# Kernel optimization log

Hardware: AMD Instinct MI355X
Metric: run time of the kernel (lower is better)

The kernel has to match this reference:

```python
import jax, jax.numpy as jnp
import numpy as np

L1 = 512
LX = 32
COUNT = 8


def setup_inputs() -> dict:
    key = jax.random.key(0)
    ks = jax.random.split(key, 9)
    B = 65536
    x = jax.random.uniform(ks[0], (B, 2 * L1), dtype=jnp.float32)  # NNUE accumulator is in [0,1]
    ls_indices = jax.random.randint(ks[1], (B,), 0, COUNT, dtype=jnp.int64)
    # params (scaled ~1/sqrt(fan_in))
    w_fact = jax.random.normal(ks[2], (LX, 2 * L1), dtype=jnp.float32) * (1.0 / np.sqrt(2 * L1))
    w0 = jax.random.normal(ks[3], (LX * COUNT, 2 * L1), dtype=jnp.float32) * (1.0 / np.sqrt(2 * L1))
    b0 = jax.random.normal(ks[4], (LX * COUNT,), dtype=jnp.float32) * 0.05
    w1 = jax.random.normal(ks[5], (LX * COUNT, LX), dtype=jnp.float32) * (1.0 / np.sqrt(LX))
    b1 = jax.random.normal(ks[6], (LX * COUNT,), dtype=jnp.float32) * 0.05
    w2 = jax.random.normal(ks[7], (1 * COUNT, LX), dtype=jnp.float32) * (1.0 / np.sqrt(LX))
    b2 = jax.random.normal(ks[8], (1 * COUNT,), dtype=jnp.float32) * 0.05
    return {"x": x, "ls_indices": ls_indices, "w_fact": w_fact,
            "w0": w0, "b0": b0, "w1": w1, "b1": b1, "w2": w2, "b2": b2}


def _stack_linear_gather(h, w, b, idx, out_dim):
    # dense Linear for all COUNT buckets, then gather the selected bucket per row
    y = (h @ w.T + b).reshape(-1, COUNT, out_dim)          # [B, COUNT, out_dim]
    return y.reshape(-1, out_dim)[idx]                      # [B, out_dim]


def reference(x, ls_indices, w_fact, w0, b0, w1, b1, w2, b2):
    B = x.shape[0]
    idx = ls_indices.astype(jnp.int32) + jnp.arange(B, dtype=jnp.int32) * COUNT
    l1f = x @ w_fact.T                                      # [B, LX]
    h = _stack_linear_gather(x, w0, b0, idx, LX) + l1f      # layer 0 + factorized term
    h = jnp.clip(h, 0.0, 1.0)
    h = _stack_linear_gather(h, w1, b1, idx, LX)            # hidden layer 1
    h = jnp.clip(h, 0.0, 1.0)
    out = _stack_linear_gather(h, w2, b2, idx, 1)           # output layer (no clamp)
    return out
```

## Files before the change

kernel.cpp:

```cpp
#include <hip/hip_runtime.h>


#define B_ROWS 65536
#define LK     1024
#define TILE   32
#define MAIN_BLOCKS (B_ROWS / TILE + 8)
#define SROW   2056

#define SORTED_OFF 1024
#define WB_OFF     (1024 + 131072)

typedef short  short8  __attribute__((ext_vector_type(8)));
typedef float  f32x16  __attribute__((ext_vector_type(16)));

__device__ __forceinline__ unsigned pkbf(float a, float b) {
    unsigned ua = __float_as_uint(a), ub = __float_as_uint(b);
    ua = (ua + 0x7FFFu + ((ua >> 16) & 1u)) >> 16;
    ub = (ub + 0x7FFFu + ((ub >> 16) & 1u)) >> 16;
    return (ua & 0xFFFFu) | (ub << 16);
}

__device__ __forceinline__ bool detect_i64(const int* p) {
    int acc = 0;
#pragma unroll
    for (int i = 0; i < 64; ++i) acc |= p[2 * i + 1];
    return acc == 0;
}

__device__ __forceinline__ int load_bucket(const int* p, int r, bool i64) {
    return (i64 ? p[2 * r] : p[r]) & 7;
}

__global__ __launch_bounds__(1024) void k_prep(
    const int* __restrict__ idx, const float* __restrict__ w0,
    const float* __restrict__ wf, uint4* __restrict__ wB,
    unsigned short* __restrict__ sorted, int* __restrict__ hdr)
{
    int t = threadIdx.x;

    if (blockIdx.x > 0) {
        int f = (blockIdx.x - 1) * 1024 + t;
        int b   = f >> 12;
        int i12 = f & 4095;
        int kc  = i12 >> 8;
        int i8  = i12 & 255;
        int n   = i8 & 31;
        int khi = i8 >> 5;
        int k = kc * 64 + khi * 8;
        const float* p0 = w0 + (size_t)(b * 32 + n) * LK + k;
        const float* pf = wf + (size_t)n * LK + k;
        float v[8];
#pragma unroll
        for (int j = 0; j < 8; ++j) v[j] = p0[j] + pf[j];
        uint4 o;
        o.x = pkbf(v[0], v[1]); o.y = pkbf(v[2], v[3]);
        o.z = pkbf(v[4], v[5]); o.w = pkbf(v[6], v[7]);
        wB[f] = o;
        return;
    }

    __shared__ int wcnt[16][8];
    __shared__ int wbase[16][8];
    __shared__ int segb[8];

    bool i64 = detect_i64(idx);
    int wv = t >> 6, lane = t & 63;
    int rowbase = wv * 4096;

    unsigned nib[8] = {0, 0, 0, 0, 0, 0, 0, 0};
    int c[8] = {0, 0, 0, 0, 0, 0, 0, 0};
#pragma unroll 8
    for (int i = 0; i < 64; ++i) {
        int r = rowbase + i * 64 + lane;
        int b = load_bucket(idx, r, i64);
        nib[i >> 3] |= (unsigned)b << (4 * (i & 7));
#pragma unroll
        for (int bb = 0; bb < 8; ++bb) c[bb] += (b == bb) ? 1 : 0;
    }
#pragma unroll
    for (int bb = 0; bb < 8; ++bb) {
        int v = c[bb];
#pragma unroll
        for (int s = 1; s < 64; s <<= 1) v += __shfl_xor(v, s);
        if (lane == 0) wcnt[wv][bb] = v;
    }
    __syncthreads();

    if (t == 0) {
        int base = 0, tt = 0;
        for (int b = 0; b < 8; ++b) {
            int tot = 0;
            for (int w = 0; w < 16; ++w) tot += wcnt[w][b];
            hdr[b] = tot; hdr[16 + b] = base; hdr[24 + b] = tt;
            segb[b] = base;
            base += tot;
            tt += (tot + TILE - 1) / TILE;
        }
        hdr[24 + 8] = tt;
    }
    __syncthreads();

    if (t < 128) {
        int w2 = t >> 3, b = t & 7;
        int base = segb[b];
        for (int w = 0; w < w2; ++w) base += wcnt[w][b];
        wbase[w2][b] = base;
    }
    __syncthreads();

    int mycur = (lane < 8) ? wbase[wv][lane] : 0;
#pragma unroll
    for (int i = 0; i < 64; ++i) {
        int b = (nib[i >> 3] >> (4 * (i & 7))) & 7;
        unsigned long long mown = 0;
        int addc = 0;
#pragma unroll
        for (int bb = 0; bb < 8; ++bb) {
            unsigned long long m = __ballot(b == bb);
            if (b == bb) mown = m;
            if (lane == bb) addc = __popcll(m);
        }
        int base = __shfl(mycur, b);
        int rank = __popcll(mown & ((1ull << lane) - 1ull));
        sorted[base + rank] = (unsigned short)(rowbase + i * 64 + lane);
        mycur += addc;
    }
}

__global__ __launch_bounds__(256, 2) void k_main(
    const float* __restrict__ x, const unsigned short* __restrict__ sorted,
    const int* __restrict__ hdr, const uint4* __restrict__ wB,
    const float* __restrict__ b0, const float* __restrict__ w1,
    const float* __restrict__ b1, const float* __restrict__ w2,
    const float* __restrict__ b2, float* __restrict__ out)
{
    __shared__ __align__(16) unsigned char smem[TILE * SROW];
    float* rbuf = (float*)smem;
    float* hb   = (float*)(smem + 16384);

    int total = hdr[24 + 8];
    int g = blockIdx.x;
    if (g >= total) return;

    int bkt = 0;
    while (bkt < 7 && hdr[24 + bkt + 1] <= g) bkt++;
    int tile  = g - hdr[24 + bkt];
    int cnt   = hdr[bkt];
    int seg   = hdr[16 + bkt];
    int p0    = seg + tile * TILE;
    int nrows = min(TILE, cnt - tile * TILE);

    int t    = threadIdx.x;
    int lane = t & 63;
    int wv   = t >> 6;

#pragma unroll
    for (int j0 = 0; j0 < 32; j0 += 8) {
        float4 v[8];
#pragma unroll
        for (int jj = 0; jj < 8; ++jj) {
            int j = j0 + jj;
            int gr = (int)sorted[p0 + min(j, nrows - 1)];
            v[jj] = ((const float4*)(x + (size_t)gr * LK))[t];
        }
#pragma unroll
        for (int jj = 0; jj < 8; ++jj) {
            int j = j0 + jj;
            uint2 o;
            o.x = pkbf(v[jj].x, v[jj].y);
            o.y = pkbf(v[jj].z, v[jj].w);
            *(uint2*)(smem + j * SROW + t * 8) = o;
        }
    }
    __syncthreads();

    const uint4* wBg = wB + (size_t)bkt * 4096;
    const unsigned char* Abase = smem + (size_t)(lane & 31) * SROW + 16 * (lane >> 5);

    f32x16 acc;
#pragma unroll
    for (int i = 0; i < 16; ++i) acc[i] = 0.0f;

    union UA { uint2 h[2]; short8 s; };
    union UB { uint4 u;    short8 s; };
#pragma unroll
    for (int cc = 0; cc < 16; ++cc) {
        int c = wv * 16 + cc;
        UA ua;
        ua.h[0] = *(const uint2*)(Abase + 32 * c);
        ua.h[1] = *(const uint2*)(Abase + 32 * c + 8);
        UB ub;
        ub.u = wBg[c * 64 + lane];
        acc = __builtin_amdgcn_mfma_f32_32x32x16_bf16(ua.s, ub.s, acc, 0, 0, 0);
    }

    __syncthreads();
#pragma unroll
    for (int r = 0; r < 16; ++r)
        rbuf[wv * 1024 + r * 64 + lane] = acc[r];
    __syncthreads();

#pragma unroll
    for (int q = 0; q < 4; ++q) {
        int e = t + 256 * q;
        float s = rbuf[e] + rbuf[1024 + e] + rbuf[2048 + e] + rbuf[3072 + e];
        int rr = e >> 6, ll = e & 63;
        int m = (rr & 3) + 8 * (rr >> 2) + 4 * (ll >> 5);
        int n = ll & 31;
        float h = s + b0[bkt * 32 + n];
        h = fminf(fmaxf(h, 0.0f), 1.0f);
        hb[m * 36 + n] = h;
    }
    __syncthreads();

    if (t < 64) {
        int r = t >> 1, half = t & 1;
        const float4* hr = (const float4*)(hb + r * 36);
        float4 ha[8];
#pragma unroll
        for (int q = 0; q < 8; ++q) ha[q] = hr[q];
        const float* w1b = w1 + (size_t)bkt * 1024;
        const float* b1b = b1 + bkt * 32;
        const float* w2b = w2 + bkt * 32;
        float partial = 0.0f;
#pragma unroll
        for (int jj = 0; jj < 16; ++jj) {
            int j2 = half * 16 + jj;
            const float4* wr = (const float4*)&w1b[j2 * 32];
            float s = b1b[j2];
#pragma unroll
            for (int q = 0; q < 8; ++q) {
                float4 w4 = wr[q];
                s += ha[q].x * w4.x + ha[q].y * w4.y + ha[q].z * w4.z + ha[q].w * w4.w;
            }
            s = fminf(fmaxf(s, 0.0f), 1.0f);
            partial += s * w2b[j2];
        }
        partial += __shfl_xor(partial, 1);
        if (half == 0 && r < nrows) {
            int gr = (int)sorted[p0 + r];
            out[gr] = partial + b2[bkt];
        }
    }
}

extern "C" void kernel_launch(void* const* d_in, const int* in_sizes, int n_in,
                              void* d_out, int out_size, void* d_ws, size_t ws_size,
                              hipStream_t stream) {
    const float* x   = (const float*)d_in[0];
    const int*   lsi = (const int*)  d_in[1];
    const float* wf  = (const float*)d_in[2];
    const float* w0  = (const float*)d_in[3];
    const float* b0  = (const float*)d_in[4];
    const float* w1  = (const float*)d_in[5];
    const float* b1  = (const float*)d_in[6];
    const float* w2  = (const float*)d_in[7];
    const float* b2  = (const float*)d_in[8];
    float* out = (float*)d_out;

    char* ws = (char*)d_ws;
    int* hdr = (int*)ws;
    unsigned short* sorted = (unsigned short*)(ws + SORTED_OFF);
    uint4* wB = (uint4*)(ws + WB_OFF);

    k_prep<<<33, 1024, 0, stream>>>(lsi, w0, wf, wB, sorted, hdr);
    k_main<<<MAIN_BLOCKS, 256, 0, stream>>>(x, sorted, hdr, wB,
                                            b0, w1, b1, w2, b2, out);
}
```

Measured before the change: 434.3 us.

## Compute all eight buckets densely per tile instead of sorting rows by bucket

Drops the bucket sort and the indirect row gather. Each block now reads 32 contiguous rows and computes layer 0 for all eight buckets, with each wave handling two buckets over the full K range, so no cross-wave reduction is needed. The per-row bucket then selects which hidden vector feeds the small tail layers, and the tail is spread over all 256 threads instead of 64. This removes the sort pass, the scattered loads and the split-K reduction, at the cost of roughly eight times more MFMA work and more weight reads per block.

```diff
diff --git a/kernel.cpp b/kernel.cpp
--- a/kernel.cpp
+++ b/kernel.cpp
@@ -4,11 +4,8 @@
 #define B_ROWS 65536
 #define LK     1024
 #define TILE   32
-#define MAIN_BLOCKS (B_ROWS / TILE + 8)
+#define NBLK   (B_ROWS / TILE)
 #define SROW   2056
-
-#define SORTED_OFF 1024
-#define WB_OFF     (1024 + 131072)
 
 typedef short  short8  __attribute__((ext_vector_type(8)));
 typedef float  f32x16  __attribute__((ext_vector_type(16)));
@@ -32,216 +29,127 @@
 }
 
 __global__ __launch_bounds__(1024) void k_prep(
-    const int* __restrict__ idx, const float* __restrict__ w0,
-    const float* __restrict__ wf, uint4* __restrict__ wB,
-    unsigned short* __restrict__ sorted, int* __restrict__ hdr)
+    const float* __restrict__ w0, const float* __restrict__ wf,
+    uint4* __restrict__ wB)
 {
-    int t = threadIdx.x;
-
-    if (blockIdx.x > 0) {
-        int f = (blockIdx.x - 1) * 1024 + t;
-        int b   = f >> 12;
-        int i12 = f & 4095;
-        int kc  = i12 >> 8;
-        int i8  = i12 & 255;
-        int n   = i8 & 31;
-        int khi = i8 >> 5;
-        int k = kc * 64 + khi * 8;
-        const float* p0 = w0 + (size_t)(b * 32 + n) * LK + k;
-        const float* pf = wf + (size_t)n * LK + k;
-        float v[8];
+    int f = blockIdx.x * 1024 + threadIdx.x;
+    int b   = f >> 12;
+    int i12 = f & 4095;
+    int kc  = i12 >> 8;
+    int i8  = i12 & 255;
+    int n   = i8 & 31;
+    int khi = i8 >> 5;
+    int k = kc * 64 + khi * 8;
+    const float* p0 = w0 + (size_t)(b * 32 + n) * LK + k;
+    const float* pf = wf + (size_t)n * LK + k;
+    float v[8];
 #pragma unroll
-        for (int j = 0; j < 8; ++j) v[j] = p0[j] + pf[j];
-        uint4 o;
-        o.x = pkbf(v[0], v[1]); o.y = pkbf(v[2], v[3]);
-        o.z = pkbf(v[4], v[5]); o.w = pkbf(v[6], v[7]);
-        wB[f] = o;
-        return;
-    }
-
-    __shared__ int wcnt[16][8];
-    __shared__ int wbase[16][8];
-    __shared__ int segb[8];
-
-    bool i64 = detect_i64(idx);
-    int wv = t >> 6, lane = t & 63;
-    int rowbase = wv * 4096;
-
-    unsigned nib[8] = {0, 0, 0, 0, 0, 0, 0, 0};
-    int c[8] = {0, 0, 0, 0, 0, 0, 0, 0};
-#pragma unroll 8
-    for (int i = 0; i < 64; ++i) {
-        int r = rowbase + i * 64 + lane;
-        int b = load_bucket(idx, r, i64);
-        nib[i >> 3] |= (unsigned)b << (4 * (i & 7));
-#pragma unroll
-        for (int bb = 0; bb < 8; ++bb) c[bb] += (b == bb) ? 1 : 0;
-    }
-#pragma unroll
-    for (int bb = 0; bb < 8; ++bb) {
-        int v = c[bb];
-#pragma unroll
-        for (int s = 1; s < 64; s <<= 1) v += __shfl_xor(v, s);
-        if (lane == 0) wcnt[wv][bb] = v;
-    }
-    __syncthreads();
-
-    if (t == 0) {
-        int base = 0, tt = 0;
-        for (int b = 0; b < 8; ++b) {
-            int tot = 0;
-            for (int w = 0; w < 16; ++w) tot += wcnt[w][b];
-            hdr[b] = tot; hdr[16 + b] = base; hdr[24 + b] = tt;
-            segb[b] = base;
-            base += tot;
-            tt += (tot + TILE - 1) / TILE;
-        }
-        hdr[24 + 8] = tt;
-    }
-    __syncthreads();
-
-    if (t < 128) {
-        int w2 = t >> 3, b = t & 7;
-        int base = segb[b];
-        for (int w = 0; w < w2; ++w) base += wcnt[w][b];
-        wbase[w2][b] = base;
-    }
-    __syncthreads();
-
-    int mycur = (lane < 8) ? wbase[wv][lane] : 0;
-#pragma unroll
-    for (int i = 0; i < 64; ++i) {
-        int b = (nib[i >> 3] >> (4 * (i & 7))) & 7;
-        unsigned long long mown = 0;
-        int addc = 0;
-#pragma unroll
-        for (int bb = 0; bb < 8; ++bb) {
-            unsigned long long m = __ballot(b == bb);
-            if (b == bb) mown = m;
-            if (lane == bb) addc = __popcll(m);
-        }
-        int base = __shfl(mycur, b);
-        int rank = __popcll(mown & ((1ull << lane) - 1ull));
-        sorted[base + rank] = (unsigned short)(rowbase + i * 64 + lane);
-        mycur += addc;
-    }
+    for (int j = 0; j < 8; ++j) v[j] = p0[j] + pf[j];
+    uint4 o;
+    o.x = pkbf(v[0], v[1]); o.y = pkbf(v[2], v[3]);
+    o.z = pkbf(v[4], v[5]); o.w = pkbf(v[6], v[7]);
+    wB[f] = o;
 }
 
 __global__ __launch_bounds__(256, 2) void k_main(
-    const float* __restrict__ x, const unsigned short* __restrict__ sorted,
-    const int* __restrict__ hdr, const uint4* __restrict__ wB,
+    const float* __restrict__ x, const int* __restrict__ idx,
+    const uint4* __restrict__ wB,
     const float* __restrict__ b0, const float* __restrict__ w1,
     const float* __restrict__ b1, const float* __restrict__ w2,
     const float* __restrict__ b2, float* __restrict__ out)
 {
     __shared__ __align__(16) unsigned char smem[TILE * SROW];
-    float* rbuf = (float*)smem;
-    float* hb   = (float*)(smem + 16384);
+    float* hb = (float*)smem;
 
-    int total = hdr[24 + 8];
-    int g = blockIdx.x;
-    if (g >= total) return;
-
-    int bkt = 0;
-    while (bkt < 7 && hdr[24 + bkt + 1] <= g) bkt++;
-    int tile  = g - hdr[24 + bkt];
-    int cnt   = hdr[bkt];
-    int seg   = hdr[16 + bkt];
-    int p0    = seg + tile * TILE;
-    int nrows = min(TILE, cnt - tile * TILE);
-
+    int g    = blockIdx.x;
+    int row0 = g * TILE;
     int t    = threadIdx.x;
     int lane = t & 63;
     int wv   = t >> 6;
 
+    const float4* src = (const float4*)(x + (size_t)row0 * LK);
 #pragma unroll
     for (int j0 = 0; j0 < 32; j0 += 8) {
         float4 v[8];
 #pragma unroll
-        for (int jj = 0; jj < 8; ++jj) {
-            int j = j0 + jj;
-            int gr = (int)sorted[p0 + min(j, nrows - 1)];
-            v[jj] = ((const float4*)(x + (size_t)gr * LK))[t];
-        }
+        for (int jj = 0; jj < 8; ++jj)
+            v[jj] = src[(j0 + jj) * 256 + t];
 #pragma unroll
         for (int jj = 0; jj < 8; ++jj) {
-            int j = j0 + jj;
             uint2 o;
             o.x = pkbf(v[jj].x, v[jj].y);
             o.y = pkbf(v[jj].z, v[jj].w);
-            *(uint2*)(smem + j * SROW + t * 8) = o;
+            *(uint2*)(smem + (j0 + jj) * SROW + t * 8) = o;
         }
     }
     __syncthreads();
 
-    const uint4* wBg = wB + (size_t)bkt * 4096;
-    const unsigned char* Abase = smem + (size_t)(lane & 31) * SROW + 16 * (lane >> 5);
+    const unsigned char* Ab = smem + (size_t)(lane & 31) * SROW + 16 * (lane >> 5);
+    const uint4* wB0 = wB + (size_t)(2 * wv) * 4096;
+    const uint4* wB1 = wB0 + 4096;
 
-    f32x16 acc;
+    f32x16 acc0, acc1;
 #pragma unroll
-    for (int i = 0; i < 16; ++i) acc[i] = 0.0f;
+    for (int i = 0; i < 16; ++i) { acc0[i] = 0.0f; acc1[i] = 0.0f; }
 
     union UA { uint2 h[2]; short8 s; };
     union UB { uint4 u;    short8 s; };
-#pragma unroll
-    for (int cc = 0; cc < 16; ++cc) {
-        int c = wv * 16 + cc;
+#pragma unroll 4
+    for (int c = 0; c < 64; ++c) {
         UA ua;
-        ua.h[0] = *(const uint2*)(Abase + 32 * c);
-        ua.h[1] = *(const uint2*)(Abase + 32 * c + 8);
-        UB ub;
-        ub.u = wBg[c * 64 + lane];
-        acc = __builtin_amdgcn_mfma_f32_32x32x16_bf16(ua.s, ub.s, acc, 0, 0, 0);
+        ua.h[0] = *(const uint2*)(Ab + 32 * c);
+        ua.h[1] = *(const uint2*)(Ab + 32 * c + 8);
+        UB u0, u1;
+        u0.u = wB0[c * 64 + lane];
+        u1.u = wB1[c * 64 + lane];
+        acc0 = __builtin_amdgcn_mfma_f32_32x32x16_bf16(ua.s, u0.s, acc0, 0, 0, 0);
+        acc1 = __builtin_amdgcn_mfma_f32_32x32x16_bf16(ua.s, u1.s, acc1, 0, 0, 0);
     }
-
-    __syncthreads();
-#pragma unroll
-    for (int r = 0; r < 16; ++r)
-        rbuf[wv * 1024 + r * 64 + lane] = acc[r];
     __syncthreads();
 
 #pragma unroll
-    for (int q = 0; q < 4; ++q) {
-        int e = t + 256 * q;
-        float s = rbuf[e] + rbuf[1024 + e] + rbuf[2048 + e] + rbuf[3072 + e];
-        int rr = e >> 6, ll = e & 63;
-        int m = (rr & 3) + 8 * (rr >> 2) + 4 * (ll >> 5);
-        int n = ll & 31;
-        float h = s + b0[bkt * 32 + n];
-        h = fminf(fmaxf(h, 0.0f), 1.0f);
-        hb[m * 36 + n] = h;
+    for (int pp = 0; pp < 2; ++pp) {
+        int bk = 2 * wv + pp;
+        float bv = b0[bk * 32 + (lane & 31)];
+#pragma unroll
+        for (int r = 0; r < 16; ++r) {
+            int m = (r & 3) + 8 * (r >> 2) + 4 * (lane >> 5);
+            float h = (pp ? acc1[r] : acc0[r]) + bv;
+            h = fminf(fmaxf(h, 0.0f), 1.0f);
+            hb[bk * 1152 + m * 36 + (lane & 31)] = h;
+        }
     }
     __syncthreads();
 
-    if (t < 64) {
-        int r = t >> 1, half = t & 1;
-        const float4* hr = (const float4*)(hb + r * 36);
-        float4 ha[8];
+    bool i64 = detect_i64(idx);
+    int r   = t >> 3;
+    int sub = t & 7;
+    int bk  = load_bucket(idx, row0 + r, i64);
+    const float4* hr = (const float4*)(hb + bk * 1152 + r * 36);
+    float4 ha[8];
 #pragma unroll
-        for (int q = 0; q < 8; ++q) ha[q] = hr[q];
-        const float* w1b = w1 + (size_t)bkt * 1024;
-        const float* b1b = b1 + bkt * 32;
-        const float* w2b = w2 + bkt * 32;
-        float partial = 0.0f;
+    for (int q = 0; q < 8; ++q) ha[q] = hr[q];
+    const float* w1b = w1 + (size_t)bk * 1024;
+    const float* b1b = b1 + bk * 32;
+    const float* w2b = w2 + bk * 32;
+    float partial = 0.0f;
 #pragma unroll
-        for (int jj = 0; jj < 16; ++jj) {
-            int j2 = half * 16 + jj;
-            const float4* wr = (const float4*)&w1b[j2 * 32];
-            float s = b1b[j2];
+    for (int jj = 0; jj < 4; ++jj) {
+        int j2 = sub * 4 + jj;
+        const float4* wr = (const float4*)&w1b[j2 * 32];
+        float s = b1b[j2];
 #pragma unroll
-            for (int q = 0; q < 8; ++q) {
-                float4 w4 = wr[q];
-                s += ha[q].x * w4.x + ha[q].y * w4.y + ha[q].z * w4.z + ha[q].w * w4.w;
-            }
-            s = fminf(fmaxf(s, 0.0f), 1.0f);
-            partial += s * w2b[j2];
+        for (int q = 0; q < 8; ++q) {
+            float4 w4 = wr[q];
+            s += ha[q].x * w4.x + ha[q].y * w4.y + ha[q].z * w4.z + ha[q].w * w4.w;
         }
-        partial += __shfl_xor(partial, 1);
-        if (half == 0 && r < nrows) {
-            int gr = (int)sorted[p0 + r];
-            out[gr] = partial + b2[bkt];
-        }
+        s = fminf(fmaxf(s, 0.0f), 1.0f);
+        partial += s * w2b[j2];
     }
+    partial += __shfl_xor(partial, 1);
+    partial += __shfl_xor(partial, 2);
+    partial += __shfl_xor(partial, 4);
+    if (sub == 0) out[row0 + r] = partial + b2[bk];
 }
 
 extern "C" void kernel_launch(void* const* d_in, const int* in_sizes, int n_in,
@@ -258,12 +166,8 @@
     const float* b2  = (const float*)d_in[8];
     float* out = (float*)d_out;
 
-    char* ws = (char*)d_ws;
-    int* hdr = (int*)ws;
-    unsigned short* sorted = (unsigned short*)(ws + SORTED_OFF);
-    uint4* wB = (uint4*)(ws + WB_OFF);
+    uint4* wB = (uint4*)d_ws;
 
-    k_prep<<<33, 1024, 0, stream>>>(lsi, w0, wf, wB, sorted, hdr);
-    k_main<<<MAIN_BLOCKS, 256, 0, stream>>>(x, sorted, hdr, wB,
-                                            b0, w1, b1, w2, b2, out);
+    k_prep<<<32, 1024, 0, stream>>>(w0, wf, wB);
+    k_main<<<NBLK, 256, 0, stream>>>(x, lsi, wB, b0, w1, b1, w2, b2, out);
 }
```

New measurement: 450.2 us. 3.6% more time.
